# Performance work log

Hardware: AMD Instinct MI355X
Metric: run time of the kernel (lower is better)

Reference implementation:

```python
import jax, jax.numpy as jnp
import numpy as np

N_NODES = 50000
N_EDGES = 1_600_000
IN_F = 128
OUT_F = 32
HEADS = 4
EDGE_F = 4
EDGE_HID = 32


def setup_inputs() -> dict:
    key = jax.random.key(0)
    ks = jax.random.split(key, 12)
    x = jax.random.normal(ks[0], (N_NODES, IN_F), dtype=jnp.float32)
    edge_index = jax.random.randint(ks[1], (2, N_EDGES), 0, N_NODES, dtype=jnp.int32)
    edge_attr = jax.random.normal(ks[2], (N_EDGES, EDGE_F), dtype=jnp.float32)
    # linear: in_features -> heads*out_features (stored as [in, out] for x @ W)
    W = jax.random.normal(ks[3], (IN_F, HEADS * OUT_F), dtype=jnp.float32) * (1.0 / np.sqrt(IN_F))
    b = jnp.zeros((HEADS * OUT_F,), dtype=jnp.float32)
    # edge_proj: Linear(EDGE_F,32) -> ReLU -> Linear(32, heads)
    eW1 = jax.random.normal(ks[4], (EDGE_F, EDGE_HID), dtype=jnp.float32) * (1.0 / np.sqrt(EDGE_F))
    eb1 = jnp.zeros((EDGE_HID,), dtype=jnp.float32)
    eW2 = jax.random.normal(ks[5], (EDGE_HID, HEADS), dtype=jnp.float32) * (1.0 / np.sqrt(EDGE_HID))
    eb2 = jnp.zeros((HEADS,), dtype=jnp.float32)
    att_src = jax.random.normal(ks[6], (1, HEADS, OUT_F), dtype=jnp.float32) * 0.1
    att_dst = jax.random.normal(ks[7], (1, HEADS, OUT_F), dtype=jnp.float32) * 0.1
    return {"x": x, "edge_index": edge_index, "edge_attr": edge_attr,
            "W": W, "b": b, "eW1": eW1, "eb1": eb1, "eW2": eW2, "eb2": eb2,
            "att_src": att_src, "att_dst": att_dst}


def reference(x, edge_index, edge_attr, W, b, eW1, eb1, eW2, eb2, att_src, att_dst):
    N = x.shape[0]
    src, dst = edge_index[0], edge_index[1]
    E = src.shape[0]

    h = (x @ W + b).reshape(N, HEADS, OUT_F)                     # [N,H,F]
    alpha_src = jnp.sum(h[src] * att_src, axis=-1)               # [E,H]
    alpha_dst = jnp.sum(h[dst] * att_dst, axis=-1)               # [E,H]
    edge_att = jax.nn.relu(edge_attr @ eW1 + eb1) @ eW2 + eb2    # [E,H]
    alpha = jax.nn.leaky_relu(alpha_src + alpha_dst + edge_att, negative_slope=0.2)

    # softmax_by_src: dense [N,H] buffer of -inf, scatter-set by src
    # softmax over the NODE axis, then gather back per edge.
    last = jax.ops.segment_max(jnp.arange(E, dtype=jnp.int32), src, num_segments=N)  # [N]
    valid = last >= 0
    dense = jnp.where(valid[:, None], alpha[jnp.clip(last, 0)], -jnp.inf)  # [N,H]
    dense = jax.nn.softmax(dense, axis=0)
    alpha_e = dense[src]                                         # [E,H]

    # dropout: module default training=False path (identity), eval mode
    # scatter-add aggregation: out[src] += h[dst] * alpha_e (all heads at once)
    msg = h[dst] * alpha_e[:, :, None]                           # [E,H,F]
    out = jnp.zeros_like(h).at[src].add(msg)                     # [N,H,F]
    return out.mean(axis=1)                                      # [N,F]
```

## Files before the change

kernel.cpp:

```cpp
#include <hip/hip_runtime.h>
#include <hip/hip_fp16.h>
#include <math.h>


#define SUPCAP 9216
#define AGG_CAP 2048
#define BIN_CHUNK 2048

__global__ __launch_bounds__(256, 4) void k_gemm(
    const float* __restrict__ x, const float* __restrict__ W,
    const float* __restrict__ b, const float* __restrict__ att_src,
    const float* __restrict__ att_dst, __half* __restrict__ hbuf16,
    float* __restrict__ s_, float* __restrict__ t_, int N) {
  __shared__ __align__(16) float xs[32 * 132];
  __shared__ __align__(16) float ws[32 * 132];
  int tx = threadIdx.x;
  int r0 = blockIdx.x * 32;
  const float4* xg = (const float4*)(x + (size_t)r0 * 128);
#pragma unroll
  for (int j = 0; j < 4; ++j) {
    int l = tx + j * 256;
    int row = l >> 5, col4 = l & 31;
    float4 v = make_float4(0.f, 0.f, 0.f, 0.f);
    if (r0 + row < N) v = xg[l];
    *(float4*)(xs + row * 132 + col4 * 4) = v;
  }
  int cg = tx & 15, rg = tx >> 4;
  float acc[2][8];
#pragma unroll
  for (int r = 0; r < 2; ++r)
#pragma unroll
    for (int c = 0; c < 8; ++c) acc[r][c] = 0.f;
  const float4* Wg4 = (const float4*)W;
  const float* xbase = xs + rg * 2 * 132;
  int woff = cg * 8 + ((cg >> 3) << 2);
  for (int kt = 0; kt < 4; ++kt) {
    __syncthreads();
#pragma unroll
    for (int j = 0; j < 4; ++j) {
      int ll = tx + j * 256;
      int row = ll >> 5, c4 = ll & 31;
      *(float4*)(ws + row * 132 + c4 * 4 + ((c4 >> 4) << 2)) = Wg4[kt * 1024 + ll];
    }
    __syncthreads();
#pragma unroll 2
    for (int k4 = 0; k4 < 8; ++k4) {
      float4 xr0 = *(const float4*)(xbase + kt * 32 + k4 * 4);
      float4 xr1 = *(const float4*)(xbase + 132 + kt * 32 + k4 * 4);
#pragma unroll
      for (int kk = 0; kk < 4; ++kk) {
        const float* wrow = ws + (k4 * 4 + kk) * 132 + woff;
        float4 w0 = *(const float4*)(wrow);
        float4 w1 = *(const float4*)(wrow + 4);
        const float wc[8] = {w0.x, w0.y, w0.z, w0.w, w1.x, w1.y, w1.z, w1.w};
        float xv0 = ((const float*)&xr0)[kk];
        float xv1 = ((const float*)&xr1)[kk];
#pragma unroll
        for (int c = 0; c < 8; ++c) {
          acc[0][c] += xv0 * wc[c];
          acc[1][c] += xv1 * wc[c];
        }
      }
    }
  }
  float4 b0 = ((const float4*)b)[cg * 2],       b1 = ((const float4*)b)[cg * 2 + 1];
  float4 s0 = ((const float4*)att_src)[cg * 2], s1 = ((const float4*)att_src)[cg * 2 + 1];
  float4 d0 = ((const float4*)att_dst)[cg * 2], d1 = ((const float4*)att_dst)[cg * 2 + 1];
  const float bbv[8] = {b0.x, b0.y, b0.z, b0.w, b1.x, b1.y, b1.z, b1.w};
  const float asv[8] = {s0.x, s0.y, s0.z, s0.w, s1.x, s1.y, s1.z, s1.w};
  const float adv[8] = {d0.x, d0.y, d0.z, d0.w, d1.x, d1.y, d1.z, d1.w};
  int hd = cg >> 2;
#pragma unroll
  for (int r = 0; r < 2; ++r) {
    float o[8];
#pragma unroll
    for (int c = 0; c < 8; ++c) o[c] = acc[r][c] + bbv[c];
    float sp = 0.f, tp = 0.f;
#pragma unroll
    for (int c = 0; c < 8; ++c) { sp += o[c] * asv[c]; tp += o[c] * adv[c]; }
    sp += __shfl_xor(sp, 1); sp += __shfl_xor(sp, 2);
    tp += __shfl_xor(tp, 1); tp += __shfl_xor(tp, 2);
    int grow = r0 + rg * 2 + r;
    if (grow < N) {
      __half2 h0 = __floats2half2_rn(o[0], o[1]);
      __half2 h1 = __floats2half2_rn(o[2], o[3]);
      __half2 h2 = __floats2half2_rn(o[4], o[5]);
      __half2 h3 = __floats2half2_rn(o[6], o[7]);
      uint4 u;
      u.x = *(unsigned*)&h0; u.y = *(unsigned*)&h1;
      u.z = *(unsigned*)&h2; u.w = *(unsigned*)&h3;
      ((uint4*)(hbuf16 + (size_t)grow * 128))[cg] = u;
      if ((tx & 3) == 0) {
        s_[grow * 4 + hd] = sp;
        t_[grow * 4 + hd] = tp;
      }
    }
  }
}

__global__ __launch_bounds__(256) void k_bin(
    const int* __restrict__ src, const int* __restrict__ dst,
    int* __restrict__ bcur, unsigned* __restrict__ bin_y,
    unsigned* __restrict__ bin_e, int E, int nsup) {
  __shared__ uint2 ebuf[BIN_CHUNK];
  __shared__ int hist[256], bas[256], curs[256], gpos[256];
  int tx = threadIdx.x;
  int e0 = blockIdx.x * BIN_CHUNK;
  int n = E - e0; if (n > BIN_CHUNK) n = BIN_CHUNK;
  hist[tx] = 0;
  __syncthreads();
  for (int i = tx; i < n; i += 256) {
    atomicAdd(&hist[src[e0 + i] >> 8], 1);
  }
  __syncthreads();
  int v = hist[tx];
  bas[tx] = v;
  __syncthreads();
  for (int off = 1; off < 256; off <<= 1) {
    int t = (tx >= off) ? bas[tx - off] : 0;
    __syncthreads();
    bas[tx] += t;
    __syncthreads();
  }
  curs[tx] = bas[tx] - v;
  if (tx < nsup && v > 0) gpos[tx] = atomicAdd(&bcur[tx], v);
  __syncthreads();
  for (int i = tx; i < n; i += 256) {
    int e = e0 + i;
    int s = src[e], d = dst[e];
    int pos = atomicAdd(&curs[s >> 8], 1);
    unsigned loc = (unsigned)(s & 255);
    ebuf[pos] = make_uint2((loc << 24) | (unsigned)e, (loc << 16) | (unsigned)d);
  }
  __syncthreads();
  int wave = tx >> 6, lane = tx & 63;
  for (int bb = wave; bb < nsup; bb += 4) {
    int cnt = hist[bb];
    if (cnt == 0) continue;
    int lbase = bas[bb] - cnt;
    int g = gpos[bb];
    unsigned* dpy = bin_y + (size_t)bb * SUPCAP + g;
    unsigned* dpe = bin_e + (size_t)bb * SUPCAP + g;
    for (int i = lane; i < cnt; i += 64)
      if (g + i < SUPCAP) {
        uint2 w = ebuf[lbase + i];
        dpe[i] = w.x;
        dpy[i] = w.y;
      }
  }
}

__global__ __launch_bounds__(256) void k_dense(
    const int* __restrict__ bcur, const unsigned* __restrict__ bin_e,
    const unsigned* __restrict__ bin_y,
    const int* __restrict__ dst, const float* __restrict__ edge_attr,
    const float* __restrict__ eW1, const float* __restrict__ eb1,
    const float* __restrict__ eW2, const float* __restrict__ eb2,
    const float* __restrict__ s_, const float* __restrict__ t_,
    float* __restrict__ dense, float* __restrict__ pmax,
    float* __restrict__ psum,
    unsigned short* __restrict__ sorted_dst,
    int* __restrict__ noff, int* __restrict__ ncnt, int N) {
  __shared__ int lastv[256];
  __shared__ int hist[256], bas[256], curs[256];
  __shared__ float lm[256 * 4], ls[256 * 4];
  int sp = blockIdx.x, tx = threadIdx.x;
  lastv[tx] = -1;
  hist[tx] = 0;
  __syncthreads();
  int cnt = bcur[sp]; if (cnt > SUPCAP) cnt = SUPCAP;
  const unsigned* be = bin_e + (size_t)sp * SUPCAP;
  const unsigned* by = bin_y + (size_t)sp * SUPCAP;
  for (int i = tx; i < cnt; i += 256) {
    unsigned p = be[i];
    atomicMax(&lastv[p >> 24], (int)(p & 0xFFFFFF));
    atomicAdd(&hist[by[i] >> 16], 1);
  }
  __syncthreads();
  int v = hist[tx];
  bas[tx] = v;
  __syncthreads();
  for (int off = 1; off < 256; off <<= 1) {
    int t = (tx >= off) ? bas[tx - off] : 0;
    __syncthreads();
    bas[tx] += t;
    __syncthreads();
  }
  curs[tx] = bas[tx] - v;
  int gn = sp * 256 + tx;
  noff[gn] = sp * SUPCAP + bas[tx] - v;
  ncnt[gn] = v;
  __syncthreads();
  unsigned short* sd = sorted_dst + (size_t)sp * SUPCAP;
  for (int i = tx; i < cnt; i += 256) {
    unsigned y = by[i];
    int pos = atomicAdd(&curs[y >> 16], 1);
    sd[pos] = (unsigned short)y;
  }
  float vv[4] = {-INFINITY, -INFINITY, -INFINITY, -INFINITY};
  if (gn < N) {
    int e = lastv[tx];
    if (e >= 0) {
      int d = dst[e];
      const float* ea = edge_attr + (size_t)e * 4;
      float e0 = ea[0], e1 = ea[1], e2 = ea[2], e3 = ea[3];
      float a0 = eb2[0], a1 = eb2[1], a2 = eb2[2], a3 = eb2[3];
#pragma unroll
      for (int i = 0; i < 32; ++i) {
        float hid = eb1[i] + e0 * eW1[i] + e1 * eW1[32 + i] + e2 * eW1[64 + i] + e3 * eW1[96 + i];
        hid = fmaxf(hid, 0.f);
        a0 += hid * eW2[i * 4 + 0]; a1 += hid * eW2[i * 4 + 1];
        a2 += hid * eW2[i * 4 + 2]; a3 += hid * eW2[i * 4 + 3];
      }
      float w0 = s_[gn * 4 + 0] + t_[d * 4 + 0] + a0;
      float w1 = s_[gn * 4 + 1] + t_[d * 4 + 1] + a1;
      float w2 = s_[gn * 4 + 2] + t_[d * 4 + 2] + a2;
      float w3 = s_[gn * 4 + 3] + t_[d * 4 + 3] + a3;
      vv[0] = w0 > 0.f ? w0 : 0.2f * w0;
      vv[1] = w1 > 0.f ? w1 : 0.2f * w1;
      vv[2] = w2 > 0.f ? w2 : 0.2f * w2;
      vv[3] = w3 > 0.f ? w3 : 0.2f * w3;
    }
#pragma unroll
    for (int h = 0; h < 4; ++h) dense[gn * 4 + h] = vv[h];
  }
#pragma unroll
  for (int h = 0; h < 4; ++h) {
    lm[tx * 4 + h] = vv[h];
    ls[tx * 4 + h] = (vv[h] > -INFINITY) ? 1.f : 0.f;
  }
  __syncthreads();
  for (int off = 128; off > 0; off >>= 1) {
    if (tx < off) {
#pragma unroll
      for (int h = 0; h < 4; ++h) {
        float m2 = lm[(tx + off) * 4 + h], s2 = ls[(tx + off) * 4 + h];
        float m1 = lm[tx * 4 + h], s1 = ls[tx * 4 + h];
        float M = fmaxf(m1, m2);
        if (M > -INFINITY) {
          ls[tx * 4 + h] = s1 * expf(m1 - M) + s2 * expf(m2 - M);
          lm[tx * 4 + h] = M;
        }
      }
    }
    __syncthreads();
  }
  if (tx == 0) {
#pragma unroll
    for (int h = 0; h < 4; ++h) {
      pmax[sp * 4 + h] = lm[h];
      psum[sp * 4 + h] = ls[h];
    }
  }
}

__global__ void k_smax2(const float* __restrict__ pmax, const float* __restrict__ psum,
                        int nb, float* __restrict__ gmax, float* __restrict__ ginv) {
  int tx = threadIdx.x;
  int h = tx & 3, chunk = tx >> 2;
  float m = -INFINITY, s = 0.f;
  for (int bq = chunk; bq < nb; bq += 64) {
    float m2 = pmax[bq * 4 + h], s2 = psum[bq * 4 + h];
    float M = fmaxf(m, m2);
    if (M > -INFINITY) {
      s = s * expf(m - M) + s2 * expf(m2 - M);
      m = M;
    }
  }
  __shared__ float lm[256], ls[256];
  lm[tx] = m; ls[tx] = s;
  __syncthreads();
  for (int off = 128; off >= 4; off >>= 1) {
    if (tx < off) {
      float m2 = lm[tx + off], s2 = ls[tx + off];
      float m1 = lm[tx], s1 = ls[tx];
      float M = fmaxf(m1, m2);
      if (M > -INFINITY) {
        ls[tx] = s1 * expf(m1 - M) + s2 * expf(m2 - M);
        lm[tx] = M;
      }
    }
    __syncthreads();
  }
  if (tx < 4) {
    gmax[tx] = lm[tx];
    ginv[tx] = 1.f / ls[tx];
  }
}

#define ACC(r, P, Q) { \
  float2 f0 = __half22float2(*(__half2*)&r.x), f1 = __half22float2(*(__half2*)&r.y); \
  float2 f2 = __half22float2(*(__half2*)&r.z), f3 = __half22float2(*(__half2*)&r.w); \
  P.x += f0.x; P.y += f0.y; P.z += f1.x; P.w += f1.y; \
  Q.x += f2.x; Q.y += f2.y; Q.z += f3.x; Q.w += f3.y; }

__global__ __launch_bounds__(256) void k_agg(
    const unsigned short* __restrict__ sorted_dst,
    const int* __restrict__ noff, const int* __restrict__ ncnt,
    const __half* __restrict__ hbuf16, const float* __restrict__ dense,
    const float* __restrict__ gmax, const float* __restrict__ ginv,
    float* __restrict__ out, int N) {
  __shared__ unsigned short sl[AGG_CAP];
  int tx = threadIdx.x;
  int n0 = blockIdx.x << 4;
  int nlast = n0 + 15; if (nlast > N - 1) nlast = N - 1;
  int lstart = noff[n0];
  int lend = noff[nlast] + ncnt[nlast];
  int total = lend - lstart; if (total > AGG_CAP) total = AGG_CAP;
  for (int i = tx; i < total; i += 256) sl[i] = sorted_dst[lstart + i];
  __syncthreads();
  int g = tx >> 4, l = tx & 15;
  int n = n0 + g;
  if (n >= N) return;
  int beg = noff[n] - lstart;
  int cnt = ncnt[n];
  if (beg + cnt > total) cnt = total - beg;
  int end = beg + cnt;
  int hd = l >> 2;
  float w = expf(dense[(size_t)n * 4 + hd] - gmax[hd]) * ginv[hd];
  float4 p0 = {0, 0, 0, 0}, q0 = {0, 0, 0, 0};
  float4 p1 = {0, 0, 0, 0}, q1 = {0, 0, 0, 0};
  int e = beg;
  for (; e + 7 < end; e += 8) {
    int c0 = sl[e],     c1 = sl[e + 1], c2 = sl[e + 2], c3 = sl[e + 3];
    int c4_ = sl[e + 4], c5 = sl[e + 5], c6 = sl[e + 6], c7 = sl[e + 7];
    uint4 r0 = *((const uint4*)(hbuf16 + ((size_t)c0  << 7)) + l);
    uint4 r1 = *((const uint4*)(hbuf16 + ((size_t)c1  << 7)) + l);
    uint4 r2 = *((const uint4*)(hbuf16 + ((size_t)c2  << 7)) + l);
    uint4 r3 = *((const uint4*)(hbuf16 + ((size_t)c3  << 7)) + l);
    uint4 r4 = *((const uint4*)(hbuf16 + ((size_t)c4_ << 7)) + l);
    uint4 r5 = *((const uint4*)(hbuf16 + ((size_t)c5  << 7)) + l);
    uint4 r6 = *((const uint4*)(hbuf16 + ((size_t)c6  << 7)) + l);
    uint4 r7 = *((const uint4*)(hbuf16 + ((size_t)c7  << 7)) + l);
    ACC(r0, p0, q0); ACC(r1, p1, q1); ACC(r2, p0, q0); ACC(r3, p1, q1);
    ACC(r4, p0, q0); ACC(r5, p1, q1); ACC(r6, p0, q0); ACC(r7, p1, q1);
  }
  for (; e + 3 < end; e += 4) {
    int c0 = sl[e], c1 = sl[e + 1], c2 = sl[e + 2], c3 = sl[e + 3];
    uint4 r0 = *((const uint4*)(hbuf16 + ((size_t)c0 << 7)) + l);
    uint4 r1 = *((const uint4*)(hbuf16 + ((size_t)c1 << 7)) + l);
    uint4 r2 = *((const uint4*)(hbuf16 + ((size_t)c2 << 7)) + l);
    uint4 r3 = *((const uint4*)(hbuf16 + ((size_t)c3 << 7)) + l);
    ACC(r0, p0, q0); ACC(r1, p1, q1); ACC(r2, p0, q0); ACC(r3, p1, q1);
  }
  for (; e < end; ++e) {
    int c0 = sl[e];
    uint4 r0 = *((const uint4*)(hbuf16 + ((size_t)c0 << 7)) + l);
    ACC(r0, p0, q0);
  }
  p0.x += p1.x; p0.y += p1.y; p0.z += p1.z; p0.w += p1.w;
  q0.x += q1.x; q0.y += q1.y; q0.z += q1.z; q0.w += q1.w;
  p0.x *= w; p0.y *= w; p0.z *= w; p0.w *= w;
  q0.x *= w; q0.y *= w; q0.z *= w; q0.w *= w;
  p0.x += __shfl_xor(p0.x, 4);  p0.y += __shfl_xor(p0.y, 4);
  p0.z += __shfl_xor(p0.z, 4);  p0.w += __shfl_xor(p0.w, 4);
  q0.x += __shfl_xor(q0.x, 4);  q0.y += __shfl_xor(q0.y, 4);
  q0.z += __shfl_xor(q0.z, 4);  q0.w += __shfl_xor(q0.w, 4);
  p0.x += __shfl_xor(p0.x, 8);  p0.y += __shfl_xor(p0.y, 8);
  p0.z += __shfl_xor(p0.z, 8);  p0.w += __shfl_xor(p0.w, 8);
  q0.x += __shfl_xor(q0.x, 8);  q0.y += __shfl_xor(q0.y, 8);
  q0.z += __shfl_xor(q0.z, 8);  q0.w += __shfl_xor(q0.w, 8);
  if (l < 4) {
    float4 oA, oB;
    oA.x = 0.25f * p0.x; oA.y = 0.25f * p0.y; oA.z = 0.25f * p0.z; oA.w = 0.25f * p0.w;
    oB.x = 0.25f * q0.x; oB.y = 0.25f * q0.y; oB.z = 0.25f * q0.z; oB.w = 0.25f * q0.w;
    *(float4*)(out + (size_t)n * 32 + l * 8) = oA;
    *(float4*)(out + (size_t)n * 32 + l * 8 + 4) = oB;
  }
}

extern "C" void kernel_launch(void* const* d_in, const int* in_sizes, int n_in,
                              void* d_out, int out_size, void* d_ws, size_t ws_size,
                              hipStream_t stream) {
  const float* x        = (const float*)d_in[0];
  const int*   ei       = (const int*)d_in[1];
  const float* edge_attr= (const float*)d_in[2];
  const float* W        = (const float*)d_in[3];
  const float* b        = (const float*)d_in[4];
  const float* eW1      = (const float*)d_in[5];
  const float* eb1      = (const float*)d_in[6];
  const float* eW2      = (const float*)d_in[7];
  const float* eb2      = (const float*)d_in[8];
  const float* att_src  = (const float*)d_in[9];
  const float* att_dst  = (const float*)d_in[10];
  float* out = (float*)d_out;

  const int N = in_sizes[0] / 128;
  const int E = in_sizes[1] / 2;
  const int* src = ei;
  const int* dst = ei + E;
  const int NSUP = (N + 255) >> 8;

  char* wp = (char*)d_ws;
  auto alloc = [&](size_t bytes) -> void* {
    void* p = (void*)wp;
    wp += (bytes + 255) & ~(size_t)255;
    return p;
  };
  __half* hbuf16 = (__half*)alloc((size_t)N * 128 * 2);
  float* s_    = (float*)alloc((size_t)N * 4 * 4);
  float* t_    = (float*)alloc((size_t)N * 4 * 4);
  float* dense = (float*)alloc((size_t)N * 4 * 4);
  float* pmax  = (float*)alloc((size_t)NSUP * 4 * 4);
  float* psum  = (float*)alloc((size_t)NSUP * 4 * 4);
  float* gmax  = (float*)alloc(4 * 4);
  float* ginv  = (float*)alloc(4 * 4);
  int* bcur    = (int*)alloc((size_t)NSUP * 4);
  unsigned* bin_y = (unsigned*)alloc((size_t)NSUP * SUPCAP * 4);
  unsigned* bin_e = (unsigned*)alloc((size_t)NSUP * SUPCAP * 4);
  unsigned short* sorted_dst = (unsigned short*)alloc((size_t)NSUP * SUPCAP * 2);
  int* noff    = (int*)alloc((size_t)NSUP * 256 * 4);
  int* ncnt    = (int*)alloc((size_t)NSUP * 256 * 4);

  hipMemsetAsync(bcur, 0, (size_t)NSUP * 4, stream);
  k_gemm<<<(N + 31) / 32, 256, 0, stream>>>(x, W, b, att_src, att_dst, hbuf16, s_, t_, N);
  k_bin<<<(E + BIN_CHUNK - 1) / BIN_CHUNK, 256, 0, stream>>>(src, dst, bcur, bin_y, bin_e, E, NSUP);
  k_dense<<<NSUP, 256, 0, stream>>>(bcur, bin_e, bin_y, dst, edge_attr, eW1, eb1, eW2, eb2,
                                    s_, t_, dense, pmax, psum, sorted_dst, noff, ncnt, N);
  k_smax2<<<1, 256, 0, stream>>>(pmax, psum, NSUP, gmax, ginv);
  k_agg<<<(N + 15) / 16, 256, 0, stream>>>(sorted_dst, noff, ncnt, hbuf16, dense, gmax, ginv, out, N);
}
```

Baseline: 255.2 us.

## Merge GEMM and edge-binning kernels into one interleaved horizontal launch

Fuses the independent node GEMM kernel and the edge binning kernel into a single launch. Block indices alternate between the two roles so that compute-bound GEMM tiles and memory/atomic-bound binning tiles share the GPU concurrently. Shared memory is unioned into one buffer sized for the larger role. This removes one kernel launch and the serialization between two independent stages, but gives both roles the larger shared-memory footprint, which can lower occupancy for the binning blocks.

```diff
diff --git a/kernel.cpp b/kernel.cpp
--- a/kernel.cpp
+++ b/kernel.cpp
@@ -7,146 +7,158 @@
 #define AGG_CAP 2048
 #define BIN_CHUNK 2048
 
-__global__ __launch_bounds__(256, 4) void k_gemm(
+__global__ __launch_bounds__(256, 4) void k_pre(
     const float* __restrict__ x, const float* __restrict__ W,
     const float* __restrict__ b, const float* __restrict__ att_src,
     const float* __restrict__ att_dst, __half* __restrict__ hbuf16,
-    float* __restrict__ s_, float* __restrict__ t_, int N) {
-  __shared__ __align__(16) float xs[32 * 132];
-  __shared__ __align__(16) float ws[32 * 132];
-  int tx = threadIdx.x;
-  int r0 = blockIdx.x * 32;
-  const float4* xg = (const float4*)(x + (size_t)r0 * 128);
-#pragma unroll
-  for (int j = 0; j < 4; ++j) {
-    int l = tx + j * 256;
-    int row = l >> 5, col4 = l & 31;
-    float4 v = make_float4(0.f, 0.f, 0.f, 0.f);
-    if (r0 + row < N) v = xg[l];
-    *(float4*)(xs + row * 132 + col4 * 4) = v;
-  }
-  int cg = tx & 15, rg = tx >> 4;
-  float acc[2][8];
-#pragma unroll
-  for (int r = 0; r < 2; ++r)
-#pragma unroll
-    for (int c = 0; c < 8; ++c) acc[r][c] = 0.f;
-  const float4* Wg4 = (const float4*)W;
-  const float* xbase = xs + rg * 2 * 132;
-  int woff = cg * 8 + ((cg >> 3) << 2);
-  for (int kt = 0; kt < 4; ++kt) {
-    __syncthreads();
-#pragma unroll
-    for (int j = 0; j < 4; ++j) {
-      int ll = tx + j * 256;
-      int row = ll >> 5, c4 = ll & 31;
-      *(float4*)(ws + row * 132 + c4 * 4 + ((c4 >> 4) << 2)) = Wg4[kt * 1024 + ll];
-    }
-    __syncthreads();
-#pragma unroll 2
-    for (int k4 = 0; k4 < 8; ++k4) {
-      float4 xr0 = *(const float4*)(xbase + kt * 32 + k4 * 4);
-      float4 xr1 = *(const float4*)(xbase + 132 + kt * 32 + k4 * 4);
-#pragma unroll
-      for (int kk = 0; kk < 4; ++kk) {
-        const float* wrow = ws + (k4 * 4 + kk) * 132 + woff;
-        float4 w0 = *(const float4*)(wrow);
-        float4 w1 = *(const float4*)(wrow + 4);
-        const float wc[8] = {w0.x, w0.y, w0.z, w0.w, w1.x, w1.y, w1.z, w1.w};
-        float xv0 = ((const float*)&xr0)[kk];
-        float xv1 = ((const float*)&xr1)[kk];
-#pragma unroll
-        for (int c = 0; c < 8; ++c) {
-          acc[0][c] += xv0 * wc[c];
-          acc[1][c] += xv1 * wc[c];
-        }
-      }
-    }
-  }
-  float4 b0 = ((const float4*)b)[cg * 2],       b1 = ((const float4*)b)[cg * 2 + 1];
-  float4 s0 = ((const float4*)att_src)[cg * 2], s1 = ((const float4*)att_src)[cg * 2 + 1];
-  float4 d0 = ((const float4*)att_dst)[cg * 2], d1 = ((const float4*)att_dst)[cg * 2 + 1];
-  const float bbv[8] = {b0.x, b0.y, b0.z, b0.w, b1.x, b1.y, b1.z, b1.w};
-  const float asv[8] = {s0.x, s0.y, s0.z, s0.w, s1.x, s1.y, s1.z, s1.w};
-  const float adv[8] = {d0.x, d0.y, d0.z, d0.w, d1.x, d1.y, d1.z, d1.w};
-  int hd = cg >> 2;
-#pragma unroll
-  for (int r = 0; r < 2; ++r) {
-    float o[8];
-#pragma unroll
-    for (int c = 0; c < 8; ++c) o[c] = acc[r][c] + bbv[c];
-    float sp = 0.f, tp = 0.f;
-#pragma unroll
-    for (int c = 0; c < 8; ++c) { sp += o[c] * asv[c]; tp += o[c] * adv[c]; }
-    sp += __shfl_xor(sp, 1); sp += __shfl_xor(sp, 2);
-    tp += __shfl_xor(tp, 1); tp += __shfl_xor(tp, 2);
-    int grow = r0 + rg * 2 + r;
-    if (grow < N) {
-      __half2 h0 = __floats2half2_rn(o[0], o[1]);
-      __half2 h1 = __floats2half2_rn(o[2], o[3]);
-      __half2 h2 = __floats2half2_rn(o[4], o[5]);
-      __half2 h3 = __floats2half2_rn(o[6], o[7]);
-      uint4 u;
-      u.x = *(unsigned*)&h0; u.y = *(unsigned*)&h1;
-      u.z = *(unsigned*)&h2; u.w = *(unsigned*)&h3;
-      ((uint4*)(hbuf16 + (size_t)grow * 128))[cg] = u;
-      if ((tx & 3) == 0) {
-        s_[grow * 4 + hd] = sp;
-        t_[grow * 4 + hd] = tp;
-      }
-    }
-  }
-}
-
-__global__ __launch_bounds__(256) void k_bin(
+    float* __restrict__ s_, float* __restrict__ t_,
     const int* __restrict__ src, const int* __restrict__ dst,
     int* __restrict__ bcur, unsigned* __restrict__ bin_y,
-    unsigned* __restrict__ bin_e, int E, int nsup) {
-  __shared__ uint2 ebuf[BIN_CHUNK];
-  __shared__ int hist[256], bas[256], curs[256], gpos[256];
+    unsigned* __restrict__ bin_e,
+    int N, int E, int nsup, int ngemm, int nbin) {
+  __shared__ __align__(16) float smem[8448];
   int tx = threadIdx.x;
-  int e0 = blockIdx.x * BIN_CHUNK;
-  int n = E - e0; if (n > BIN_CHUNK) n = BIN_CHUNK;
-  hist[tx] = 0;
-  __syncthreads();
-  for (int i = tx; i < n; i += 256) {
-    atomicAdd(&hist[src[e0 + i] >> 8], 1);
-  }
-  __syncthreads();
-  int v = hist[tx];
-  bas[tx] = v;
-  __syncthreads();
-  for (int off = 1; off < 256; off <<= 1) {
-    int t = (tx >= off) ? bas[tx - off] : 0;
-    __syncthreads();
-    bas[tx] += t;
-    __syncthreads();
-  }
-  curs[tx] = bas[tx] - v;
-  if (tx < nsup && v > 0) gpos[tx] = atomicAdd(&bcur[tx], v);
-  __syncthreads();
-  for (int i = tx; i < n; i += 256) {
-    int e = e0 + i;
-    int s = src[e], d = dst[e];
-    int pos = atomicAdd(&curs[s >> 8], 1);
-    unsigned loc = (unsigned)(s & 255);
-    ebuf[pos] = make_uint2((loc << 24) | (unsigned)e, (loc << 16) | (unsigned)d);
-  }
-  __syncthreads();
-  int wave = tx >> 6, lane = tx & 63;
-  for (int bb = wave; bb < nsup; bb += 4) {
-    int cnt = hist[bb];
-    if (cnt == 0) continue;
-    int lbase = bas[bb] - cnt;
-    int g = gpos[bb];
-    unsigned* dpy = bin_y + (size_t)bb * SUPCAP + g;
-    unsigned* dpe = bin_e + (size_t)bb * SUPCAP + g;
-    for (int i = lane; i < cnt; i += 64)
-      if (g + i < SUPCAP) {
-        uint2 w = ebuf[lbase + i];
-        dpe[i] = w.x;
-        dpy[i] = w.y;
-      }
+  int bid = blockIdx.x;
+  int mmin = (nbin < ngemm) ? nbin : ngemm;
+  int m2 = 2 * mmin;
+  bool isbin;
+  int wid;
+  if (bid < m2) { isbin = (bid & 1); wid = bid >> 1; }
+  else { isbin = (nbin > ngemm); wid = mmin + (bid - m2); }
+
+  if (isbin) {
+    uint2* ebuf = (uint2*)smem;
+    int* hist = (int*)(smem + 4096);
+    int* bas  = hist + 256;
+    int* curs = bas + 256;
+    int* gpos = curs + 256;
+    int e0 = wid * BIN_CHUNK;
+    int n = E - e0; if (n > BIN_CHUNK) n = BIN_CHUNK;
+    hist[tx] = 0;
+    __syncthreads();
+    for (int i = tx; i < n; i += 256) {
+      atomicAdd(&hist[src[e0 + i] >> 8], 1);
+    }
+    __syncthreads();
+    int v = hist[tx];
+    bas[tx] = v;
+    __syncthreads();
+    for (int off = 1; off < 256; off <<= 1) {
+      int t = (tx >= off) ? bas[tx - off] : 0;
+      __syncthreads();
+      bas[tx] += t;
+      __syncthreads();
+    }
+    curs[tx] = bas[tx] - v;
+    if (tx < nsup && v > 0) gpos[tx] = atomicAdd(&bcur[tx], v);
+    __syncthreads();
+    for (int i = tx; i < n; i += 256) {
+      int e = e0 + i;
+      int s = src[e], d = dst[e];
+      int pos = atomicAdd(&curs[s >> 8], 1);
+      unsigned loc = (unsigned)(s & 255);
+      ebuf[pos] = make_uint2((loc << 24) | (unsigned)e, (loc << 16) | (unsigned)d);
+    }
+    __syncthreads();
+    int wave = tx >> 6, lane = tx & 63;
+    for (int bb = wave; bb < nsup; bb += 4) {
+      int cnt = hist[bb];
+      if (cnt == 0) continue;
+      int lbase = bas[bb] - cnt;
+      int g = gpos[bb];
+      unsigned* dpy = bin_y + (size_t)bb * SUPCAP + g;
+      unsigned* dpe = bin_e + (size_t)bb * SUPCAP + g;
+      for (int i = lane; i < cnt; i += 64)
+        if (g + i < SUPCAP) {
+          uint2 w = ebuf[lbase + i];
+          dpe[i] = w.x;
+          dpy[i] = w.y;
+        }
+    }
+  } else {
+    float* xs = smem;
+    float* ws = smem + 32 * 132;
+    int r0 = wid * 32;
+    const float4* xg = (const float4*)(x + (size_t)r0 * 128);
+#pragma unroll
+    for (int j = 0; j < 4; ++j) {
+      int l = tx + j * 256;
+      int row = l >> 5, col4 = l & 31;
+      float4 v = make_float4(0.f, 0.f, 0.f, 0.f);
+      if (r0 + row < N) v = xg[l];
+      *(float4*)(xs + row * 132 + col4 * 4) = v;
+    }
+    int cg = tx & 15, rg = tx >> 4;
+    float acc[2][8];
+#pragma unroll
+    for (int r = 0; r < 2; ++r)
+#pragma unroll
+      for (int c = 0; c < 8; ++c) acc[r][c] = 0.f;
+    const float4* Wg4 = (const float4*)W;
+    const float* xbase = xs + rg * 2 * 132;
+    int woff = cg * 8 + ((cg >> 3) << 2);
+    for (int kt = 0; kt < 4; ++kt) {
+      __syncthreads();
+#pragma unroll
+      for (int j = 0; j < 4; ++j) {
+        int ll = tx + j * 256;
+        int row = ll >> 5, c4 = ll & 31;
+        *(float4*)(ws + row * 132 + c4 * 4 + ((c4 >> 4) << 2)) = Wg4[kt * 1024 + ll];
+      }
+      __syncthreads();
+#pragma unroll 2
+      for (int k4 = 0; k4 < 8; ++k4) {
+        float4 xr0 = *(const float4*)(xbase + kt * 32 + k4 * 4);
+        float4 xr1 = *(const float4*)(xbase + 132 + kt * 32 + k4 * 4);
+#pragma unroll
+        for (int kk = 0; kk < 4; ++kk) {
+          const float* wrow = ws + (k4 * 4 + kk) * 132 + woff;
+          float4 w0 = *(const float4*)(wrow);
+          float4 w1 = *(const float4*)(wrow + 4);
+          const float wc[8] = {w0.x, w0.y, w0.z, w0.w, w1.x, w1.y, w1.z, w1.w};
+          float xv0 = ((const float*)&xr0)[kk];
+          float xv1 = ((const float*)&xr1)[kk];
+#pragma unroll
+          for (int c = 0; c < 8; ++c) {
+            acc[0][c] += xv0 * wc[c];
+            acc[1][c] += xv1 * wc[c];
+          }
+        }
+      }
+    }
+    float4 b0 = ((const float4*)b)[cg * 2],       b1 = ((const float4*)b)[cg * 2 + 1];
+    float4 s0 = ((const float4*)att_src)[cg * 2], s1 = ((const float4*)att_src)[cg * 2 + 1];
+    float4 d0 = ((const float4*)att_dst)[cg * 2], d1 = ((const float4*)att_dst)[cg * 2 + 1];
+    const float bbv[8] = {b0.x, b0.y, b0.z, b0.w, b1.x, b1.y, b1.z, b1.w};
+    const float asv[8] = {s0.x, s0.y, s0.z, s0.w, s1.x, s1.y, s1.z, s1.w};
+    const float adv[8] = {d0.x, d0.y, d0.z, d0.w, d1.x, d1.y, d1.z, d1.w};
+    int hd = cg >> 2;
+#pragma unroll
+    for (int r = 0; r < 2; ++r) {
+      float o[8];
+#pragma unroll
+      for (int c = 0; c < 8; ++c) o[c] = acc[r][c] + bbv[c];
+      float sp = 0.f, tp = 0.f;
+#pragma unroll
+      for (int c = 0; c < 8; ++c) { sp += o[c] * asv[c]; tp += o[c] * adv[c]; }
+      sp += __shfl_xor(sp, 1); sp += __shfl_xor(sp, 2);
+      tp += __shfl_xor(tp, 1); tp += __shfl_xor(tp, 2);
+      int grow = r0 + rg * 2 + r;
+      if (grow < N) {
+        __half2 h0 = __floats2half2_rn(o[0], o[1]);
+        __half2 h1 = __floats2half2_rn(o[2], o[3]);
+        __half2 h2 = __floats2half2_rn(o[4], o[5]);
+        __half2 h3 = __floats2half2_rn(o[6], o[7]);
+        uint4 u;
+        u.x = *(unsigned*)&h0; u.y = *(unsigned*)&h1;
+        u.z = *(unsigned*)&h2; u.w = *(unsigned*)&h3;
+        ((uint4*)(hbuf16 + (size_t)grow * 128))[cg] = u;
+        if ((tx & 3) == 0) {
+          s_[grow * 4 + hd] = sp;
+          t_[grow * 4 + hd] = tp;
+        }
+      }
+    }
   }
 }
 
@@ -412,9 +424,13 @@
   int* noff    = (int*)alloc((size_t)NSUP * 256 * 4);
   int* ncnt    = (int*)alloc((size_t)NSUP * 256 * 4);
 
+  const int NGEMM = (N + 31) / 32;
+  const int NBIN  = (E + BIN_CHUNK - 1) / BIN_CHUNK;
+
   hipMemsetAsync(bcur, 0, (size_t)NSUP * 4, stream);
-  k_gemm<<<(N + 31) / 32, 256, 0, stream>>>(x, W, b, att_src, att_dst, hbuf16, s_, t_, N);
-  k_bin<<<(E + BIN_CHUNK - 1) / BIN_CHUNK, 256, 0, stream>>>(src, dst, bcur, bin_y, bin_e, E, NSUP);
+  k_pre<<<NGEMM + NBIN, 256, 0, stream>>>(x, W, b, att_src, att_dst, hbuf16, s_, t_,
+                                          src, dst, bcur, bin_y, bin_e,
+                                          N, E, NSUP, NGEMM, NBIN);
   k_dense<<<NSUP, 256, 0, stream>>>(bcur, bin_e, bin_y, dst, edge_attr, eW1, eb1, eW2, eb2,
                                     s_, t_, dense, pmax, psum, sorted_dst, noff, ncnt, N);
   k_smax2<<<1, 256, 0, stream>>>(pmax, psum, NSUP, gmax, ginv);
```

Result: faster. 243.7 us (-4.5%).
